# Kernel optimization log

Measured on AMD Instinct MI355X. Metric: run time of the kernel, lower is better.

The kernel has to match this reference:

```python
import jax, jax.numpy as jnp
import numpy as np

N_HEAD = 12
MIN_SIZE = 4
MAX_SIZE = 8
TOP_M = 16
ALPHA = 1.0
EPS = 1e-6
NEG_INF = -1e30


def setup_inputs() -> dict:
    key = jax.random.key(0)
    ks = jax.random.split(key, 4)
    B, T, C = 2, 512, 768
    x = jax.random.normal(ks[0], (B, T, C), jnp.float32)
    w_qkv = jax.random.normal(ks[1], (C, 3 * C), jnp.float32) * (1.0 / np.sqrt(C))
    b_qkv = jnp.zeros((3 * C,), jnp.float32)
    w_proj = jax.random.normal(ks[2], (C, C), jnp.float32) * (1.0 / np.sqrt(C))
    b_proj = jnp.zeros((C,), jnp.float32)
    gate_param = jnp.zeros((), jnp.float32)  # dpp_gate_init = 0.0 -> gate = 0.5
    return {"x": x, "w_qkv": w_qkv, "b_qkv": b_qkv, "w_proj": w_proj,
            "b_proj": b_proj, "gate_param": gate_param}


def _dpp_token(i, q_i, k, v):
    """Greedy DPP subset selection + attention for one query token.
    q_i: [hd], k/v: [T, hd]. Faithful to the torch greedy loop, vectorized
    over candidates with incremental Gram construction (scores only gate the
    discrete selection, so they are computed under stop_gradient, matching
    torch where they only feed Python comparisons)."""
    T, hd = k.shape
    kc = jax.lax.stop_gradient(k)
    qc = jax.lax.stop_gradient(q_i)
    # causal similarity, topk candidates
    sim = jnp.where(jnp.arange(T) <= i, kc @ qc, NEG_INF)
    _, topidx = jax.lax.top_k(sim, TOP_M)  # [M]
    # candidates = top-min(TOP_M, i+1) causal neighbors, excluding i itself
    cand_active = (jnp.arange(TOP_M) < jnp.minimum(TOP_M, i + 1)) & (topidx != i)
    cand_keys = kc[topidx]                              # [M, hd]
    cnorm = jnp.sum(cand_keys * cand_keys, axis=-1)     # [M]

    sel_idx = jnp.zeros((MAX_SIZE,), jnp.int32).at[0].set(i)
    sel_count = jnp.int32(1)
    # initial score: log(det([k_i.k_i]) + eps) / 1**alpha
    cur = jnp.log(jnp.dot(kc[i], kc[i]) + EPS)
    stopped = jnp.bool_(False)
    eye = jnp.eye(MAX_SIZE, dtype=jnp.float32)
    slots = jnp.arange(MAX_SIZE)

    for _ in range(MAX_SIZE - 1):
        rowmask = slots < sel_count                       # [S] current subset rows
        pos = (slots == sel_count).astype(jnp.float32)    # slot for new candidate
        Ksel = kc[sel_idx] * rowmask[:, None].astype(jnp.float32)  # [S, hd]
        G0 = Ksel @ Ksel.T                                # [S, S]
        cross = cand_keys @ Ksel.T                        # [M, S]
        # Gc[c,a,b] = G0[a,b] + pos[a]*cross[c,b] + pos[b]*cross[c,a] + pos[a]pos[b]*cnorm[c]
        Gc = (G0[None]
              + pos[None, :, None] * cross[:, None, :]
              + pos[None, None, :] * cross[:, :, None]
              + (pos[:, None] * pos[None, :])[None] * cnorm[:, None, None])
        newmask = rowmask | (slots == sel_count)
        # identity-pad unused rows/cols so det equals det of the active submatrix
        Gc = Gc + (eye * (1.0 - newmask.astype(jnp.float32)))[None]
        dets = jnp.linalg.det(Gc)                         # [M] (float32, as torch)
        size = (sel_count + 1).astype(jnp.float32)
        score = jnp.log(dets + EPS) / size ** ALPHA       # minimize_det=False
        masked = jnp.where(cand_active, score, NEG_INF)
        best = jnp.argmax(masked)
        best_score = masked[best]
        any_cand = jnp.any(cand_active)
        take = any_cand & (~stopped) & ((best_score > cur) | (sel_count < MIN_SIZE))
        sel_idx = jnp.where(take, sel_idx.at[sel_count].set(topidx[best].astype(jnp.int32)), sel_idx)
        cand_active = jnp.where(take, cand_active.at[best].set(False), cand_active)
        cur = jnp.where(take, best_score, cur)
        sel_count = sel_count + take.astype(jnp.int32)
        stopped = stopped | (~take)

    # attention over the selected subset (gradients flow through k, v, q here)
    rowmask = slots < sel_count
    Ks = k[sel_idx]
    Vs = v[sel_idx]
    logits = jnp.where(rowmask, (Ks @ q_i) / np.float32(np.sqrt(hd)), NEG_INF)
    w = jax.nn.softmax(logits)
    return w @ Vs


def _forward(x, w_qkv, b_qkv, w_proj, b_proj, gate_param):
    B, T, C = x.shape
    hd = C // N_HEAD
    qkv = x @ w_qkv + b_qkv
    q, k, v = jnp.split(qkv, 3, axis=-1)

    def heads(t):  # [B,T,C] -> [B*NH, T, hd]
        return t.reshape(B, T, N_HEAD, hd).transpose(0, 2, 1, 3).reshape(B * N_HEAD, T, hd)

    q, k, v = heads(q), heads(k), heads(v)

    # standard causal softmax attention (flash path, dropout=0 at eval)
    scale = np.float32(1.0 / np.sqrt(hd))
    att = jnp.einsum('nqd,nkd->nqk', q, k) * scale
    causal = jnp.tril(jnp.ones((T, T), bool))
    att = jnp.where(causal[None], att, NEG_INF)
    y_std = jnp.einsum('nqk,nkd->nqd', jax.nn.softmax(att, axis=-1), v)

    # DPP greedy-selection attention, vmapped over tokens and (batch*head)
    dpp_head = jax.vmap(_dpp_token, in_axes=(0, 0, None, None))
    y_dpp = jax.vmap(lambda qh, kh, vh: dpp_head(jnp.arange(T), qh, kh, vh))(q, k, v)

    gate = jax.nn.sigmoid(gate_param)
    y = gate * y_dpp + (1.0 - gate) * y_std
    y = y.reshape(B, N_HEAD, T, hd).transpose(0, 2, 1, 3).reshape(B, T, C)
    return y @ w_proj + b_proj


def reference(x, w_qkv, b_qkv, w_proj, b_proj, gate_param):
    return _forward(x, w_qkv, b_qkv, w_proj, b_proj, gate_param)
```

## Files before the change

kernel.cpp:

```cpp
#include <hip/hip_runtime.h>
#include <math.h>

constexpr int SEQ   = 512;
constexpr int HDIM  = 64;
constexpr int NHEAD = 12;
constexpr int NBATCH = 2;
constexpr int CDIM  = 768;
constexpr int TOPM  = 16;
constexpr int SMAX  = 8;
constexpr float NEGINF = -1e30f;

__global__ __launch_bounds__(256) void qkv_gemm_kernel(
    const float* __restrict__ x, const float* __restrict__ w,
    float* __restrict__ partial)
{
    __shared__ float As[64][36];
    __shared__ float Bs[32][68];
    const int bm = blockIdx.y * 64;
    const int bn = blockIdx.x * 64;
    const int kbase = blockIdx.z * 192;
    const int tid = threadIdx.x;
    const int tm = (tid >> 4) << 2;
    const int tn = (tid & 15) << 2;
    const int alm = tid >> 2;
    const int alk = (tid & 3) << 3;
    const int blk = tid >> 3;
    const int bln = (tid & 7) << 3;
    float acc[4][4] = {};
    for (int t = 0; t < 6; ++t) {
        const int k0 = kbase + t * 32;
        float4 a0 = *(const float4*)(x + (bm + alm) * CDIM + k0 + alk);
        float4 a1 = *(const float4*)(x + (bm + alm) * CDIM + k0 + alk + 4);
        float4 b0 = *(const float4*)(w + (k0 + blk) * (3 * CDIM) + bn + bln);
        float4 b1 = *(const float4*)(w + (k0 + blk) * (3 * CDIM) + bn + bln + 4);
        *(float4*)&As[alm][alk] = a0;
        *(float4*)&As[alm][alk + 4] = a1;
        *(float4*)&Bs[blk][bln] = b0;
        *(float4*)&Bs[blk][bln + 4] = b1;
        __syncthreads();
        #pragma unroll
        for (int k4 = 0; k4 < 8; ++k4) {
            float4 a0r = *(const float4*)&As[tm + 0][k4 << 2];
            float4 a1r = *(const float4*)&As[tm + 1][k4 << 2];
            float4 a2r = *(const float4*)&As[tm + 2][k4 << 2];
            float4 a3r = *(const float4*)&As[tm + 3][k4 << 2];
            float ar[4][4] = {{a0r.x, a0r.y, a0r.z, a0r.w},
                              {a1r.x, a1r.y, a1r.z, a1r.w},
                              {a2r.x, a2r.y, a2r.z, a2r.w},
                              {a3r.x, a3r.y, a3r.z, a3r.w}};
            #pragma unroll
            for (int j = 0; j < 4; ++j) {
                float4 b4 = *(const float4*)&Bs[(k4 << 2) + j][tn];
                float bb[4] = {b4.x, b4.y, b4.z, b4.w};
                #pragma unroll
                for (int u = 0; u < 4; ++u)
                    #pragma unroll
                    for (int w2 = 0; w2 < 4; ++w2)
                        acc[u][w2] = fmaf(ar[u][j], bb[w2], acc[u][w2]);
            }
        }
        __syncthreads();
    }
    float* dst = partial + (size_t)blockIdx.z * (1024 * 2304);
    #pragma unroll
    for (int u = 0; u < 4; ++u) {
        float4 o = {acc[u][0], acc[u][1], acc[u][2], acc[u][3]};
        *(float4*)(dst + (size_t)(bm + tm + u) * 2304 + bn + tn) = o;
    }
}

__global__ __launch_bounds__(256) void qkv_reduce_kernel(
    const float* __restrict__ partial, const float* __restrict__ bias,
    float* __restrict__ q, float* __restrict__ k, float* __restrict__ v)
{
    const int idx = blockIdx.x * 256 + threadIdx.x;
    const int m = idx / 576;
    const int cc = (idx - m * 576) << 2;
    const size_t MN = (size_t)1024 * 2304;
    float4 p0 = *(const float4*)(partial + (size_t)m * 2304 + cc);
    float4 p1 = *(const float4*)(partial + MN + (size_t)m * 2304 + cc);
    float4 p2 = *(const float4*)(partial + 2 * MN + (size_t)m * 2304 + cc);
    float4 p3 = *(const float4*)(partial + 3 * MN + (size_t)m * 2304 + cc);
    float4 b4 = *(const float4*)(bias + cc);
    float4 o = {((p0.x + p1.x) + p2.x) + p3.x + b4.x,
                ((p0.y + p1.y) + p2.y) + p3.y + b4.y,
                ((p0.z + p1.z) + p2.z) + p3.z + b4.z,
                ((p0.w + p1.w) + p2.w) + p3.w + b4.w};
    const int part = cc / CDIM;
    const int c2 = cc - part * CDIM;
    const int h = c2 >> 6, d = c2 & 63;
    const int b_ = m >> 9, t = m & 511;
    float* dst = (part == 0) ? q : ((part == 1) ? k : v);
    *(float4*)(dst + ((((size_t)b_ * NHEAD + h) * SEQ) + t) * HDIM + d) = o;
}

__global__ __launch_bounds__(256) void qkkt_kernel(
    const float* __restrict__ q, const float* __restrict__ k,
    float* __restrict__ S, float* __restrict__ KKT)
{
    __shared__ float Qs[64][68];
    __shared__ float Ka[64][68];
    __shared__ float Kb[64][68];
    const int e = blockIdx.x;
    const int n = blockIdx.y;
    int it = 0, start = 0;
    while (start + it + 1 <= e) { start += it + 1; ++it; }
    const int jt = e - start;
    const int tid = threadIdx.x;
    const float* qh = q + (size_t)n * SEQ * HDIM;
    const float* kh = k + (size_t)n * SEQ * HDIM;

    #pragma unroll
    for (int l = 0; l < 4; ++l) {
        int idx = tid + l * 256;
        int tok = idx >> 4, d4 = (idx & 15) << 2;
        *(float4*)&Qs[tok][d4] = *(const float4*)(qh + (it * 64 + tok) * HDIM + d4);
        *(float4*)&Ka[tok][d4] = *(const float4*)(kh + (it * 64 + tok) * HDIM + d4);
        *(float4*)&Kb[tok][d4] = *(const float4*)(kh + (jt * 64 + tok) * HDIM + d4);
    }
    __syncthreads();

    const int tm = (tid >> 4) << 2;
    const int tn = (tid & 15) << 2;
    float sacc[4][4] = {};
    float gacc[4][4] = {};
    #pragma unroll 4
    for (int d4 = 0; d4 < 16; ++d4) {
        float4 qr[4], ar[4], br[4];
        #pragma unroll
        for (int u = 0; u < 4; ++u) {
            qr[u] = *(const float4*)&Qs[tm + u][d4 << 2];
            ar[u] = *(const float4*)&Ka[tm + u][d4 << 2];
        }
        #pragma unroll
        for (int w2 = 0; w2 < 4; ++w2)
            br[w2] = *(const float4*)&Kb[tn + w2][d4 << 2];
        #pragma unroll
        for (int u = 0; u < 4; ++u)
            #pragma unroll
            for (int w2 = 0; w2 < 4; ++w2) {
                float s = sacc[u][w2];
                s = fmaf(qr[u].x, br[w2].x, s);
                s = fmaf(qr[u].y, br[w2].y, s);
                s = fmaf(qr[u].z, br[w2].z, s);
                s = fmaf(qr[u].w, br[w2].w, s);
                sacc[u][w2] = s;
                float g = gacc[u][w2];
                g = fmaf(ar[u].x, br[w2].x, g);
                g = fmaf(ar[u].y, br[w2].y, g);
                g = fmaf(ar[u].z, br[w2].z, g);
                g = fmaf(ar[u].w, br[w2].w, g);
                gacc[u][w2] = g;
            }
    }
    float* gdst = KKT + ((size_t)n * 36 + e) * 4096;
    #pragma unroll
    for (int u = 0; u < 4; ++u) {
        int i = it * 64 + tm + u;
        float4 o = {sacc[u][0], sacc[u][1], sacc[u][2], sacc[u][3]};
        *(float4*)(S + ((size_t)n * SEQ + i) * SEQ + jt * 64 + tn) = o;
        float4 g = {gacc[u][0], gacc[u][1], gacc[u][2], gacc[u][3]};
        *(float4*)(gdst + (tm + u) * 64 + tn) = g;
    }
}

__device__ inline double hybrid_log(double a)
{
    a = fmax(a, 1e-300);
    unsigned long long b = __double_as_longlong(a);
    int e2 = (int)((b >> 52) & 0x7FF) - 1022;
    double m = __longlong_as_double((b & 0x000FFFFFFFFFFFFFULL) |
                                    0x3FE0000000000000ULL);
    return ((double)__log2f((float)m) + (double)e2) * 0.6931471805599453;
}

#define CSW(a, b)                                                        \
    {                                                                    \
        bool sw = (v##a < v##b) || ((v##a == v##b) && (j##a > j##b));    \
        float tf = sw ? v##b : v##a;                                     \
        float uf = sw ? v##a : v##b;                                     \
        int ti = sw ? j##b : j##a;                                       \
        int ui = sw ? j##a : j##b;                                       \
        v##a = tf; v##b = uf; j##a = ti; j##b = ui;                      \
    }

__global__ __launch_bounds__(128) void dpp_kernel(
    const float* __restrict__ v, float* __restrict__ S,
    const float* __restrict__ KKT, const float* __restrict__ gate_p,
    float* __restrict__ y, float* __restrict__ denomArr)
{
    const int tid  = threadIdx.x;
    const int wid  = tid >> 6;
    const int lane = tid & 63;
    const int i = blockIdx.x * 2 + wid;
    const int n = blockIdx.y;
    const float* vh = v + (size_t)n * SEQ * HDIM;
    const float* KKTh = KKT + (size_t)n * 36 * 4096;
    float* Srow = S + ((size_t)n * SEQ + i) * SEQ;

    __shared__ float prow[2][SEQ];
    __shared__ float gramf[2][17][17];
    __shared__ int   eidx[2][17];

    float sim8[8];
    #pragma unroll
    for (int m = 0; m < 8; ++m) {
        int j = lane + (m << 6);
        sim8[m] = (j <= i) ? Srow[j] : NEGINF;
    }

    {
        float v0 = sim8[0], v1 = sim8[1], v2 = sim8[2], v3 = sim8[3],
              v4 = sim8[4], v5 = sim8[5], v6 = sim8[6], v7 = sim8[7];
        int j0 = lane, j1 = lane + 64, j2 = lane + 128, j3 = lane + 192,
            j4 = lane + 256, j5 = lane + 320, j6 = lane + 384, j7 = lane + 448;
        CSW(0, 1) CSW(2, 3) CSW(4, 5) CSW(6, 7)
        CSW(0, 2) CSW(1, 3) CSW(4, 6) CSW(5, 7)
        CSW(1, 2) CSW(5, 6)
        CSW(0, 4) CSW(1, 5) CSW(2, 6) CSW(3, 7)
        CSW(2, 4) CSW(3, 5)
        CSW(1, 2) CSW(3, 4) CSW(5, 6)

        if (lane == 0) eidx[wid][0] = i;
        #pragma unroll
        for (int s = 0; s < TOPM; ++s) {
            float rv = v0;
            #pragma unroll
            for (int off = 32; off; off >>= 1)
                rv = fmaxf(rv, __shfl_xor(rv, off));
            unsigned long long tied = __ballot(v0 == rv);
            int ri;
            if (__popcll(tied) == 1) {
                ri = __shfl(j0, (int)__builtin_ctzll(tied));
            } else {
                int cnd = (v0 == rv) ? j0 : 0x7FFFFFFF;
                #pragma unroll
                for (int off = 32; off; off >>= 1)
                    cnd = min(cnd, __shfl_xor(cnd, off));
                ri = cnd;
            }
            if (lane == 0) eidx[wid][1 + s] = ri;
            if (v0 == rv && j0 == ri) {
                v0 = v1; j0 = j1; v1 = v2; j1 = j2; v2 = v3; j2 = j3;
                v3 = v4; j3 = j4; v4 = v5; j4 = j5; v5 = v6; j5 = j6;
                v6 = v7; j6 = j7; v7 = -3e38f; j7 = 1023;
            }
        }
    }

    const float scale = 0.125f;
    float lm = -3e38f;
    #pragma unroll
    for (int m = 0; m < 8; ++m) lm = fmaxf(lm, sim8[m]);
    #pragma unroll
    for (int off = 32; off; off >>= 1) lm = fmaxf(lm, __shfl_xor(lm, off));
    const float mx = lm * scale;
    float sum = 0.f;
    #pragma unroll
    for (int m = 0; m < 8; ++m) {
        float p = expf(sim8[m] * scale - mx);
        int j = lane + (m << 6);
        prow[wid][j] = p;
        Srow[j] = p;
        sum += p;
    }
    #pragma unroll
    for (int off = 32; off; off >>= 1) sum += __shfl_xor(sum, off);
    const float denom = sum;
    asm volatile("s_waitcnt lgkmcnt(0)" ::: "memory");

    for (int e = lane; e < 153; e += 64) {
        int a = 0, st = 0;
        while (st + a + 1 <= e) { st += a + 1; ++a; }
        int b = e - st;
        int ra = eidx[wid][a], rb = eidx[wid][b];
        int row = ra > rb ? ra : rb;
        int col = ra > rb ? rb : ra;
        int itt = row >> 6, jtt = col >> 6;
        int p = ((itt * (itt + 1)) >> 1) + jtt;
        float s = KKTh[((size_t)p * 64 + (row & 63)) * 64 + (col & 63)];
        gramf[wid][a][b] = s;
        gramf[wid][b][a] = s;
    }
    asm volatile("s_waitcnt lgkmcnt(0)" ::: "memory");

    int selI[SMAX];
    int sc = 1;
    {
        const int c = lane;
        const bool isCand = (c < TOPM);
        const int nvalid = (i + 1 < TOPM) ? (i + 1) : TOPM;
        bool active = isCand && (c < nvalid) && (eidx[wid][1 + c] != i);
        double zc[7];
        #pragma unroll
        for (int t = 0; t < 7; ++t) zc[t] = 0.0;
        double det = (double)gramf[wid][0][0];
        double cur = 0.0;
        double L00 = sqrt(det > 0.0 ? det : 1e-30);
        double dcv = 0.0;
        if (isCand) {
            zc[0] = (double)gramf[wid][1 + c][0] / L00;
            dcv = (double)gramf[wid][1 + c][1 + c] - zc[0] * zc[0];
        }
        #pragma unroll
        for (int t = 0; t < SMAX; ++t) selI[t] = i;

        for (int it2 = 0; it2 < SMAX - 1; ++it2) {
            double argc = det * dcv + 1e-6;
            double key = active ? (argc > 0.0 ? argc : 1e300) : -1.0;
            int rc = c;
            #pragma unroll
            for (int off = 1; off <= 8; off <<= 1) {
                double ov = __shfl_xor(key, off);
                int    oc = __shfl_xor(rc, off);
                if (ov > key || (ov == key && oc < rc)) { key = ov; rc = oc; }
            }
            rc = __shfl(rc, 0);
            bool any = (__any(active ? 1 : 0) != 0);
            double dbest = __shfl(dcv, rc);
            bool take;
            if (it2 < 2) {
                take = any;
            } else {
                double argb = det * dbest + 1e-6;
                bool pos = argb > 0.0;
                double score = hybrid_log(pos ? argb : 1.0) / (double)(sc + 1);
                take = any && (it2 < 3 || (pos && score > cur));
                if (take) cur = pos ? score : __builtin_nan("");
            }
            if (!take) break;

            double Lss = sqrt(dbest > 1e-30 ? dbest : 1e-30);
            double zb[7];
            #pragma unroll
            for (int t = 0; t < 7; ++t) zb[t] = __shfl(zc[t], rc);
            if (isCand) {
                double crossn = (double)gramf[wid][1 + c][1 + rc];
                double s2 = 0.0;
                #pragma unroll
                for (int t = 0; t < 7; ++t) if (t < sc) s2 += zc[t] * zb[t];
                double znew = (crossn - s2) / Lss;
                #pragma unroll
                for (int t = 0; t < 7; ++t) if (t == sc) zc[t] = znew;
                dcv -= znew * znew;
            }
            det = det * dbest;
            if (c == rc) active = false;
            int newIdx = eidx[wid][1 + rc];
            #pragma unroll
            for (int t = 0; t < SMAX; ++t) if (t == sc) selI[t] = newIdx;
            ++sc;
        }
    }

    float wsum = 0.f;
    #pragma unroll
    for (int s = 0; s < SMAX; ++s) if (s < sc) wsum += prow[wid][selI[s]];
    float yd = 0.f;
    #pragma unroll
    for (int s = 0; s < SMAX; ++s)
        if (s < sc) yd = fmaf(prow[wid][selI[s]], vh[selI[s] * HDIM + lane], yd);
    const float gp = gate_p[0];
    const float gate = 1.f / (1.f + expf(-gp));
    y[((size_t)n * SEQ + i) * HDIM + lane] = gate * yd / wsum;
    if (lane == 0) denomArr[n * SEQ + i] = denom;
}

__global__ __launch_bounds__(256) void pv_gemm_kernel(
    const float* __restrict__ P, const float* __restrict__ v,
    const float* __restrict__ denomArr, const float* __restrict__ gate_p,
    float* __restrict__ y)
{
    __shared__ float Ps[64][36];
    __shared__ float Vs[32][68];
    const int tt = blockIdx.x;
    const int n  = blockIdx.y;
    const int t0 = tt * 64;
    const int tid = threadIdx.x;
    const float* Ph = P + (size_t)n * SEQ * SEQ;
    const float* vh = v + (size_t)n * SEQ * HDIM;
    const int tm = (tid >> 4) << 2;
    const int tn = (tid & 15) << 2;
    float acc[4][4] = {};
    const int jmax = t0 + 64;
    for (int j0 = 0; j0 < jmax; j0 += 32) {
        #pragma unroll
        for (int l = 0; l < 2; ++l) {
            int idx = tid + l * 256;
            int tok = idx >> 3, j4 = (idx & 7) << 2;
            *(float4*)&Ps[tok][j4] =
                *(const float4*)(Ph + (t0 + tok) * SEQ + j0 + j4);
        }
        #pragma unroll
        for (int l = 0; l < 2; ++l) {
            int idx = tid + l * 256;
            int j = idx >> 4, d4 = (idx & 15) << 2;
            *(float4*)&Vs[j][d4] = *(const float4*)(vh + (j0 + j) * HDIM + d4);
        }
        __syncthreads();
        #pragma unroll
        for (int j4 = 0; j4 < 8; ++j4) {
            float4 p0r = *(const float4*)&Ps[tm + 0][j4 << 2];
            float4 p1r = *(const float4*)&Ps[tm + 1][j4 << 2];
            float4 p2r = *(const float4*)&Ps[tm + 2][j4 << 2];
            float4 p3r = *(const float4*)&Ps[tm + 3][j4 << 2];
            float pr[4][4] = {{p0r.x, p0r.y, p0r.z, p0r.w},
                              {p1r.x, p1r.y, p1r.z, p1r.w},
                              {p2r.x, p2r.y, p2r.z, p2r.w},
                              {p3r.x, p3r.y, p3r.z, p3r.w}};
            #pragma unroll
            for (int l = 0; l < 4; ++l) {
                float4 v4 = *(const float4*)&Vs[(j4 << 2) + l][tn];
                float vv[4] = {v4.x, v4.y, v4.z, v4.w};
                #pragma unroll
                for (int u = 0; u < 4; ++u)
                    #pragma unroll
                    for (int w2 = 0; w2 < 4; ++w2)
                        acc[u][w2] = fmaf(pr[u][l], vv[w2], acc[u][w2]);
            }
        }
        __syncthreads();
    }
    const float gp = gate_p[0];
    const float gate = 1.f / (1.f + expf(-gp));
    #pragma unroll
    for (int u = 0; u < 4; ++u) {
        int i = t0 + tm + u;
        float den = denomArr[n * SEQ + i];
        #pragma unroll
        for (int w2 = 0; w2 < 4; ++w2) {
            int d = tn + w2;
            size_t off = ((size_t)n * SEQ + i) * HDIM + d;
            y[off] += (1.f - gate) * acc[u][w2] / den;
        }
    }
}

__global__ __launch_bounds__(256) void proj_gemm_kernel(
    const float* __restrict__ y, const float* __restrict__ w,
    float* __restrict__ partial)
{
    __shared__ float As[64][36];
    __shared__ float Bs[32][68];
    const int bm = blockIdx.y * 64;
    const int bn = blockIdx.x * 64;
    const int kbase = blockIdx.z * 96;
    const int tid = threadIdx.x;
    const int tm = (tid >> 4) << 2;
    const int tn = (tid & 15) << 2;
    const int alm = tid >> 2;
    const int alk = (tid & 3) << 3;
    const int blk = tid >> 3;
    const int bln = (tid & 7) << 3;
    const int row = bm + alm;
    const int b_ = row >> 9, tk = row & 511;
    const float* ybase = y + (((size_t)b_ * NHEAD) * SEQ + tk) * HDIM;

    float acc[4][4] = {};
    for (int t = 0; t < 3; ++t) {
        const int k0 = kbase + t * 32;
        int col0 = k0 + alk;
        int h0 = col0 >> 6, d0 = col0 & 63;
        float4 a0 = *(const float4*)(ybase + (size_t)h0 * SEQ * HDIM + d0);
        int col1 = col0 + 4;
        int h1 = col1 >> 6, d1 = col1 & 63;
        float4 a1 = *(const float4*)(ybase + (size_t)h1 * SEQ * HDIM + d1);
        float4 b0 = *(const float4*)(w + (k0 + blk) * CDIM + bn + bln);
        float4 b1 = *(const float4*)(w + (k0 + blk) * CDIM + bn + bln + 4);
        *(float4*)&As[alm][alk] = a0;
        *(float4*)&As[alm][alk + 4] = a1;
        *(float4*)&Bs[blk][bln] = b0;
        *(float4*)&Bs[blk][bln + 4] = b1;
        __syncthreads();
        #pragma unroll
        for (int k4 = 0; k4 < 8; ++k4) {
            float4 a0r = *(const float4*)&As[tm + 0][k4 << 2];
            float4 a1r = *(const float4*)&As[tm + 1][k4 << 2];
            float4 a2r = *(const float4*)&As[tm + 2][k4 << 2];
            float4 a3r = *(const float4*)&As[tm + 3][k4 << 2];
            float ar[4][4] = {{a0r.x, a0r.y, a0r.z, a0r.w},
                              {a1r.x, a1r.y, a1r.z, a1r.w},
                              {a2r.x, a2r.y, a2r.z, a2r.w},
                              {a3r.x, a3r.y, a3r.z, a3r.w}};
            #pragma unroll
            for (int j = 0; j < 4; ++j) {
                float4 b4 = *(const float4*)&Bs[(k4 << 2) + j][tn];
                float bb[4] = {b4.x, b4.y, b4.z, b4.w};
                #pragma unroll
                for (int u = 0; u < 4; ++u)
                    #pragma unroll
                    for (int w2 = 0; w2 < 4; ++w2)
                        acc[u][w2] = fmaf(ar[u][j], bb[w2], acc[u][w2]);
            }
        }
        __syncthreads();
    }
    float* dst = partial + (size_t)blockIdx.z * (1024 * 768);
    #pragma unroll
    for (int u = 0; u < 4; ++u) {
        float4 o = {acc[u][0], acc[u][1], acc[u][2], acc[u][3]};
        *(float4*)(dst + (size_t)(bm + tm + u) * 768 + bn + tn) = o;
    }
}

__global__ __launch_bounds__(256) void proj_reduce_kernel(
    const float* __restrict__ partial, const float* __restrict__ bias,
    float* __restrict__ out)
{
    const int idx = blockIdx.x * 256 + threadIdx.x;
    const int m = idx / 192;
    const int cc = (idx - m * 192) << 2;
    const size_t MN = (size_t)1024 * 768;
    float4 s = *(const float4*)(partial + (size_t)m * 768 + cc);
    #pragma unroll
    for (int z = 1; z < 8; ++z) {
        float4 p = *(const float4*)(partial + (size_t)z * MN + (size_t)m * 768 + cc);
        s.x += p.x; s.y += p.y; s.z += p.z; s.w += p.w;
    }
    float4 b4 = *(const float4*)(bias + cc);
    float4 o = {s.x + b4.x, s.y + b4.y, s.z + b4.z, s.w + b4.w};
    *(float4*)(out + (size_t)m * 768 + cc) = o;
}

extern "C" void kernel_launch(void* const* d_in, const int* in_sizes, int n_in,
                              void* d_out, int out_size, void* d_ws, size_t ws_size,
                              hipStream_t stream)
{
    const float* x      = (const float*)d_in[0];
    const float* w_qkv  = (const float*)d_in[1];
    const float* b_qkv  = (const float*)d_in[2];
    const float* w_proj = (const float*)d_in[3];
    const float* b_proj = (const float*)d_in[4];
    const float* gate_p = (const float*)d_in[5];
    float* out = (float*)d_out;

    float* ws = (float*)d_ws;
    const size_t HS = (size_t)NBATCH * NHEAD * SEQ * HDIM;
    const size_t SS = (size_t)NBATCH * NHEAD * SEQ * SEQ;
    float* q   = ws;
    float* k   = q + HS;
    float* v   = k + HS;
    float* y   = v + HS;
    float* S   = y + HS;
    float* den = S + SS;
    float* KKT = den + 16384;

    qkv_gemm_kernel<<<dim3((3 * CDIM) / 64, (NBATCH * SEQ) / 64, 4), 256, 0, stream>>>(
        x, w_qkv, S);
    qkv_reduce_kernel<<<2304, 256, 0, stream>>>(S, b_qkv, q, k, v);
    qkkt_kernel<<<dim3(36, NBATCH * NHEAD), 256, 0, stream>>>(q, k, S, KKT);
    dpp_kernel<<<dim3(SEQ / 2, NBATCH * NHEAD), 128, 0, stream>>>(
        v, S, KKT, gate_p, y, den);
    pv_gemm_kernel<<<dim3(SEQ / 64, NBATCH * NHEAD), 256, 0, stream>>>(
        S, v, den, gate_p, y);
    proj_gemm_kernel<<<dim3(CDIM / 64, (NBATCH * SEQ) / 64, 8), 256, 0, stream>>>(
        y, w_proj, S);
    proj_reduce_kernel<<<768, 256, 0, stream>>>(S, b_proj, out);
}
```

Measured before the change: 195.6 us.

## Shrink PV GEMM tiles, use rsqrt in DPP Cholesky, store selections in LDS

The PV GEMM tile drops from 64 to 32 query rows, which doubles the block count to fill more CUs and trims causal work per tile. The DPP kernel replaces double sqrt plus division with a float rsqrt refined by one Newton step. It also computes the triangular index in closed form instead of with a loop, removes the clamp in the log helper, and keeps the selected indices in shared memory rather than in a dynamically indexed register array. The rsqrt path costs some precision, and the unmasked dot product now relies on the unused zc entries being zero.

```diff
diff --git a/kernel.cpp b/kernel.cpp
--- a/kernel.cpp
+++ b/kernel.cpp
@@ -166,12 +166,18 @@
 
 __device__ inline double hybrid_log(double a)
 {
-    a = fmax(a, 1e-300);
     unsigned long long b = __double_as_longlong(a);
     int e2 = (int)((b >> 52) & 0x7FF) - 1022;
     double m = __longlong_as_double((b & 0x000FFFFFFFFFFFFFULL) |
                                     0x3FE0000000000000ULL);
     return ((double)__log2f((float)m) + (double)e2) * 0.6931471805599453;
+}
+
+__device__ inline double rsqrt64(double x)
+{
+    double r = (double)rsqrtf((float)x);
+    r = r * (1.5 - 0.5 * x * r * r);
+    return r;
 }
 
 #define CSW(a, b)                                                        \
@@ -201,6 +207,7 @@
     __shared__ float prow[2][SEQ];
     __shared__ float gramf[2][17][17];
     __shared__ int   eidx[2][17];
+    __shared__ int   selS[2][SMAX];
 
     float sim8[8];
     #pragma unroll
@@ -208,6 +215,7 @@
         int j = lane + (m << 6);
         sim8[m] = (j <= i) ? Srow[j] : NEGINF;
     }
+    if (lane < SMAX) selS[wid][lane] = i;
 
     {
         float v0 = sim8[0], v1 = sim8[1], v2 = sim8[2], v3 = sim8[3],
@@ -270,8 +278,10 @@
     asm volatile("s_waitcnt lgkmcnt(0)" ::: "memory");
 
     for (int e = lane; e < 153; e += 64) {
-        int a = 0, st = 0;
-        while (st + a + 1 <= e) { st += a + 1; ++a; }
+        int a = (int)((sqrtf(8.f * (float)e + 1.f) - 1.f) * 0.5f);
+        int st = (a * (a + 1)) >> 1;
+        if (st > e) { --a; st = (a * (a + 1)) >> 1; }
+        else if (st + a + 1 <= e) { ++a; st = (a * (a + 1)) >> 1; }
         int b = e - st;
         int ra = eidx[wid][a], rb = eidx[wid][b];
         int row = ra > rb ? ra : rb;
@@ -284,7 +294,6 @@
     }
     asm volatile("s_waitcnt lgkmcnt(0)" ::: "memory");
 
-    int selI[SMAX];
     int sc = 1;
     {
         const int c = lane;
@@ -296,14 +305,12 @@
         for (int t = 0; t < 7; ++t) zc[t] = 0.0;
         double det = (double)gramf[wid][0][0];
         double cur = 0.0;
-        double L00 = sqrt(det > 0.0 ? det : 1e-30);
+        double invL00 = rsqrt64(det > 0.0 ? det : 1e-30);
         double dcv = 0.0;
         if (isCand) {
-            zc[0] = (double)gramf[wid][1 + c][0] / L00;
+            zc[0] = (double)gramf[wid][1 + c][0] * invL00;
             dcv = (double)gramf[wid][1 + c][1 + c] - zc[0] * zc[0];
         }
-        #pragma unroll
-        for (int t = 0; t < SMAX; ++t) selI[t] = i;
 
         for (int it2 = 0; it2 < SMAX - 1; ++it2) {
             double argc = det * dcv + 1e-6;
@@ -330,7 +337,7 @@
             }
             if (!take) break;
 
-            double Lss = sqrt(dbest > 1e-30 ? dbest : 1e-30);
+            double invLss = rsqrt64(dbest > 1e-30 ? dbest : 1e-30);
             double zb[7];
             #pragma unroll
             for (int t = 0; t < 7; ++t) zb[t] = __shfl(zc[t], rc);
@@ -338,21 +345,22 @@
                 double crossn = (double)gramf[wid][1 + c][1 + rc];
                 double s2 = 0.0;
                 #pragma unroll
-                for (int t = 0; t < 7; ++t) if (t < sc) s2 += zc[t] * zb[t];
-                double znew = (crossn - s2) / Lss;
+                for (int t = 0; t < 7; ++t) s2 += zc[t] * zb[t];
+                double znew = (crossn - s2) * invLss;
                 #pragma unroll
                 for (int t = 0; t < 7; ++t) if (t == sc) zc[t] = znew;
                 dcv -= znew * znew;
             }
             det = det * dbest;
             if (c == rc) active = false;
-            int newIdx = eidx[wid][1 + rc];
-            #pragma unroll
-            for (int t = 0; t < SMAX; ++t) if (t == sc) selI[t] = newIdx;
+            if (lane == 0) selS[wid][sc] = eidx[wid][1 + rc];
             ++sc;
         }
     }
 
+    int selI[SMAX];
+    #pragma unroll
+    for (int s = 0; s < SMAX; ++s) selI[s] = selS[wid][s];
     float wsum = 0.f;
     #pragma unroll
     for (int s = 0; s < SMAX; ++s) if (s < sc) wsum += prow[wid][selI[s]];
@@ -371,23 +379,21 @@
     const float* __restrict__ denomArr, const float* __restrict__ gate_p,
     float* __restrict__ y)
 {
-    __shared__ float Ps[64][36];
+    __shared__ float Ps[32][36];
     __shared__ float Vs[32][68];
     const int tt = blockIdx.x;
     const int n  = blockIdx.y;
-    const int t0 = tt * 64;
+    const int t0 = tt * 32;
     const int tid = threadIdx.x;
     const float* Ph = P + (size_t)n * SEQ * SEQ;
     const float* vh = v + (size_t)n * SEQ * HDIM;
-    const int tm = (tid >> 4) << 2;
+    const int tm = (tid >> 4) << 1;
     const int tn = (tid & 15) << 2;
-    float acc[4][4] = {};
-    const int jmax = t0 + 64;
+    float acc[2][4] = {};
+    const int jmax = t0 + 32;
     for (int j0 = 0; j0 < jmax; j0 += 32) {
-        #pragma unroll
-        for (int l = 0; l < 2; ++l) {
-            int idx = tid + l * 256;
-            int tok = idx >> 3, j4 = (idx & 7) << 2;
+        {
+            int tok = tid >> 3, j4 = (tid & 7) << 2;
             *(float4*)&Ps[tok][j4] =
                 *(const float4*)(Ph + (t0 + tok) * SEQ + j0 + j4);
         }
@@ -402,18 +408,14 @@
         for (int j4 = 0; j4 < 8; ++j4) {
             float4 p0r = *(const float4*)&Ps[tm + 0][j4 << 2];
             float4 p1r = *(const float4*)&Ps[tm + 1][j4 << 2];
-            float4 p2r = *(const float4*)&Ps[tm + 2][j4 << 2];
-            float4 p3r = *(const float4*)&Ps[tm + 3][j4 << 2];
-            float pr[4][4] = {{p0r.x, p0r.y, p0r.z, p0r.w},
-                              {p1r.x, p1r.y, p1r.z, p1r.w},
-                              {p2r.x, p2r.y, p2r.z, p2r.w},
-                              {p3r.x, p3r.y, p3r.z, p3r.w}};
+            float pr[2][4] = {{p0r.x, p0r.y, p0r.z, p0r.w},
+                              {p1r.x, p1r.y, p1r.z, p1r.w}};
             #pragma unroll
             for (int l = 0; l < 4; ++l) {
                 float4 v4 = *(const float4*)&Vs[(j4 << 2) + l][tn];
                 float vv[4] = {v4.x, v4.y, v4.z, v4.w};
                 #pragma unroll
-                for (int u = 0; u < 4; ++u)
+                for (int u = 0; u < 2; ++u)
                     #pragma unroll
                     for (int w2 = 0; w2 < 4; ++w2)
                         acc[u][w2] = fmaf(pr[u][l], vv[w2], acc[u][w2]);
@@ -424,7 +426,7 @@
     const float gp = gate_p[0];
     const float gate = 1.f / (1.f + expf(-gp));
     #pragma unroll
-    for (int u = 0; u < 4; ++u) {
+    for (int u = 0; u < 2; ++u) {
         int i = t0 + tm + u;
         float den = denomArr[n * SEQ + i];
         #pragma unroll
@@ -551,7 +553,7 @@
     qkkt_kernel<<<dim3(36, NBATCH * NHEAD), 256, 0, stream>>>(q, k, S, KKT);
     dpp_kernel<<<dim3(SEQ / 2, NBATCH * NHEAD), 128, 0, stream>>>(
         v, S, KKT, gate_p, y, den);
-    pv_gemm_kernel<<<dim3(SEQ / 64, NBATCH * NHEAD), 256, 0, stream>>>(
+    pv_gemm_kernel<<<dim3(SEQ / 32, NBATCH * NHEAD), 256, 0, stream>>>(
         S, v, den, gate_p, y);
     proj_gemm_kernel<<<dim3(CDIM / 64, (NBATCH * SEQ) / 64, 8), 256, 0, stream>>>(
         y, w_proj, S);
```

Result: faster. 185.8 us (-5.1%).
